# Optimization experiments

Hardware: AMD Instinct MI355X
Metric: run time of the kernel (lower is better)

Reference implementation:

```python
import jax, jax.numpy as jnp
import numpy as np


def _gcn_norm(edge_index, num_nodes, dtype):
    # PyG GCNConv.norm: add self-loops (weight 1), symmetric deg^{-1/2} normalization
    row, col = edge_index[0], edge_index[1]
    loop = jnp.arange(num_nodes, dtype=row.dtype)
    row = jnp.concatenate([row, loop])
    col = jnp.concatenate([col, loop])
    ew = jnp.ones(row.shape[0], dtype=dtype)
    deg = jax.ops.segment_sum(ew, row, num_segments=num_nodes)
    dis = jnp.where(deg > 0, jax.lax.rsqrt(deg), 0.0)
    norm = dis[row] * ew * dis[col]
    return row, col, norm


def _masked_gcn_conv(x, row, col, norm, sigma, W, b, num_nodes):
    # mask_features: edge gather -> diff/sigma -> square -> scatter-add -> exp mask
    h = (x[col] - x[row]) / sigma            # [E, F]
    h = norm[:, None] * h * h                # [E, F]
    mask = jax.ops.segment_sum(h, row, num_segments=num_nodes)        # [N, F]
    deg = jax.ops.segment_sum(jnp.ones_like(norm), row, num_segments=num_nodes)  # degree(source), >=1 due to self-loops
    x = x * jnp.exp(-mask / deg[:, None])
    # GCNConv: linear transform then normalized aggregation source->target
    xw = x @ W                               # [N, O]
    out = jax.ops.segment_sum(norm[:, None] * xw[row], col, num_segments=num_nodes)
    return out + b


def setup_inputs() -> dict:
    key = jax.random.key(0)
    ks = jax.random.split(key, 8)
    N, E, F, H, C = 100000, 1600000, 128, 64, 40
    g = 1.414  # xavier gain used for sigma
    return {
        "x": jax.random.normal(ks[0], (N, F), jnp.float32),
        "edge_index": jax.random.randint(ks[1], (2, E), 0, N, jnp.int64),
        "sigma1": jax.random.uniform(ks[2], (1, F), jnp.float32, -1.0, 1.0) * (g * np.sqrt(6.0 / (1 + F))),
        "W1": jax.random.normal(ks[3], (F, H), jnp.float32) * (1.0 / np.sqrt(F)),
        "b1": jnp.zeros((H,), jnp.float32),
        "sigma2": jax.random.uniform(ks[4], (1, H), jnp.float32, -1.0, 1.0) * (g * np.sqrt(6.0 / (1 + H))),
        "W2": jax.random.normal(ks[5], (H, C), jnp.float32) * (1.0 / np.sqrt(H)),
        "b2": jnp.zeros((C,), jnp.float32),
    }


def reference(x, edge_index, sigma1, W1, b1, sigma2, W2, b2):
    N = x.shape[0]
    row, col, norm = _gcn_norm(edge_index, N, x.dtype)
    x = _masked_gcn_conv(x, row, col, norm, sigma1, W1, b1, N)
    x = jax.nn.relu(x)
    # dropout is identity in eval mode
    x = _masked_gcn_conv(x, row, col, norm, sigma2, W2, b2, N)
    return jax.nn.log_softmax(x, axis=1)
```

## Files before the change

kernel.cpp:

```cpp
#include <hip/hip_runtime.h>
#include <cmath>

constexpr int F1 = 128;
constexpr int H  = 64;
constexpr int NC = 40;
constexpr int NXCD = 8;

constexpr int SCAN_TPB = 256;
constexpr int SCAN_IPT = 8;
constexpr int SCAN_EPB = SCAN_TPB * SCAN_IPT;

__device__ inline unsigned short f2bf(float f) {
    union { float f; unsigned u; } v; v.f = f;
    return (unsigned short)((v.u + 0x7FFFu + ((v.u >> 16) & 1u)) >> 16);
}
__device__ inline float bflo(unsigned p) { union { float f; unsigned u; } v; v.u = p << 16; return v.f; }
__device__ inline float bfhi(unsigned p) { union { float f; unsigned u; } v; v.u = p & 0xFFFF0000u; return v.f; }
__device__ inline void unpack8(uint4 raw, float* d) {
    d[0] = bflo(raw.x); d[1] = bfhi(raw.x); d[2] = bflo(raw.y); d[3] = bfhi(raw.y);
    d[4] = bflo(raw.z); d[5] = bfhi(raw.z); d[6] = bflo(raw.w); d[7] = bfhi(raw.w);
}

__global__ void isg_kernel(const float* __restrict__ s1, float* __restrict__ i1,
                           const float* __restrict__ s2, float* __restrict__ i2) {
    int i = threadIdx.x;
    if (i < F1) i1[i] = 1.0f / s1[i];
    if (i < H)  i2[i] = 1.0f / s2[i];
}

__global__ void prep_u_kernel(const float* __restrict__ x, const float* __restrict__ isg,
                              unsigned short* __restrict__ u, size_t n8, int F) {
    size_t idx = (size_t)blockIdx.x * blockDim.x + threadIdx.x;
    if (idx >= n8) return;
    size_t base = idx * 8;
    int fk = (int)(base % (size_t)F);
    float4 a0 = *(const float4*)&x[base];
    float4 a1 = *(const float4*)&x[base + 4];
    float4 s0 = *(const float4*)&isg[fk];
    float4 s1 = *(const float4*)&isg[fk + 4];
    uint4 p;
    p.x = (unsigned)f2bf(a0.x * s0.x) | ((unsigned)f2bf(a0.y * s0.y) << 16);
    p.y = (unsigned)f2bf(a0.z * s0.z) | ((unsigned)f2bf(a0.w * s0.w) << 16);
    p.z = (unsigned)f2bf(a1.x * s1.x) | ((unsigned)f2bf(a1.y * s1.y) << 16);
    p.w = (unsigned)f2bf(a1.z * s1.z) | ((unsigned)f2bf(a1.w * s1.w) << 16);
    *(uint4*)&u[base] = p;
}

__global__ void count8_kernel(const int* __restrict__ row, const int* __restrict__ col,
                              int* __restrict__ cntO, int* __restrict__ cntI,
                              int E, int chunk, int stride) {
    int p = blockIdx.x & (NXCD - 1);
    int gid = blockIdx.x >> 3;
    unsigned lo = (unsigned)(p * chunk);
    for (int e = gid * blockDim.x + threadIdx.x; e < E; e += stride) {
        int r = row[e], c = col[e];
        if ((unsigned)r - lo < (unsigned)chunk) atomicAdd(&cntO[r], 1);
        if ((unsigned)c - lo < (unsigned)chunk) atomicAdd(&cntI[c], 1);
    }
}

__global__ void scan_partial_kernel(const int* __restrict__ cnt, int* __restrict__ bsum, int M) {
    __shared__ int red[SCAN_TPB];
    int t = threadIdx.x;
    int i0 = blockIdx.x * SCAN_EPB + t * SCAN_IPT;
    int s = 0;
#pragma unroll
    for (int k = 0; k < SCAN_IPT; ++k) {
        int i = i0 + k;
        if (i < M) s += cnt[i];
    }
    red[t] = s;
    __syncthreads();
    for (int off = SCAN_TPB / 2; off > 0; off >>= 1) {
        if (t < off) red[t] += red[t + off];
        __syncthreads();
    }
    if (t == 0) bsum[blockIdx.x] = red[0];
}

__global__ void scan_offsets_kernel(int* __restrict__ bsum, int nb,
                                    int* __restrict__ rowptrO, int* __restrict__ rowptrI,
                                    int N, int E) {
    __shared__ int sh[1024];
    int t = threadIdx.x;
    sh[t] = (t < nb) ? bsum[t] : 0;
    __syncthreads();
    for (int off = 1; off < 1024; off <<= 1) {
        int v = (t >= off) ? sh[t - off] : 0;
        __syncthreads();
        sh[t] += v;
        __syncthreads();
    }
    if (t < nb) bsum[t] = (t > 0) ? sh[t - 1] : 0;
    if (t == 0) { rowptrO[N] = E; rowptrI[N] = E; }
}

__global__ void scan_final_kernel(int* __restrict__ cntO, int* __restrict__ cntI,
                                  const int* __restrict__ bsum,
                                  int* __restrict__ rowptrO, int* __restrict__ rowptrI,
                                  float* __restrict__ dis, int N, int E) {
    __shared__ int sh[SCAN_TPB];
    int t = threadIdx.x;
    int M = 2 * N;
    const int* cnt = cntO;
    int i0 = blockIdx.x * SCAN_EPB + t * SCAN_IPT;
    int cv[SCAN_IPT], pre[SCAN_IPT];
    int run = 0;
#pragma unroll
    for (int k = 0; k < SCAN_IPT; ++k) {
        int i = i0 + k;
        cv[k] = (i < M) ? cnt[i] : 0;
        pre[k] = run;
        run += cv[k];
    }
    sh[t] = run;
    __syncthreads();
    for (int off = 1; off < SCAN_TPB; off <<= 1) {
        int v = (t >= off) ? sh[t - off] : 0;
        __syncthreads();
        sh[t] += v;
        __syncthreads();
    }
    int toff = ((t > 0) ? sh[t - 1] : 0) + bsum[blockIdx.x];
#pragma unroll
    for (int k = 0; k < SCAN_IPT; ++k) {
        int i = i0 + k;
        if (i < M) {
            int val = toff + pre[k];
            if (i < N) {
                rowptrO[i] = val;
                cntO[i] = val;
                dis[i] = rsqrtf((float)(cv[k] + 1));
            } else {
                rowptrI[i - N] = val - E;
                cntI[i - N] = val - E;
            }
        }
    }
}

__global__ void build8_kernel(const int* __restrict__ row, const int* __restrict__ col,
                              int* __restrict__ curO, int* __restrict__ curI,
                              int* __restrict__ adjO, int* __restrict__ adjI,
                              int E, int chunk, int stride) {
    int p = blockIdx.x & (NXCD - 1);
    int gid = blockIdx.x >> 3;
    unsigned lo = (unsigned)(p * chunk);
    for (int e = gid * blockDim.x + threadIdx.x; e < E; e += stride) {
        int r = row[e], c = col[e];
        if ((unsigned)r - lo < (unsigned)chunk) adjO[atomicAdd(&curO[r], 1)] = c;
        if ((unsigned)c - lo < (unsigned)chunk) adjI[atomicAdd(&curI[c], 1)] = r;
    }
}

template<int F, int O, int R>
__global__ void fused_mask_gemm_kernel(const int* __restrict__ rowptr, const int* __restrict__ adj,
                                       const float* __restrict__ dis, const float* __restrict__ x,
                                       const unsigned short* __restrict__ u,
                                       const float* __restrict__ W,
                                       unsigned short* __restrict__ Ybf, int N) {
    constexpr int NT = R * 64;
    constexpr int G = F / 8;
    constexpr int NPI = 64 / G;
    constexpr int FP = F + 4;
    __shared__ __align__(16) float WsT[O * FP];
    __shared__ __align__(16) float Xs[R][FP];
    int tid = threadIdx.x;
    for (int i = tid; i < F * O; i += NT) {
        int f = i / O, o = i - f * O;
        WsT[o * FP + f] = W[i];
    }
    int w = tid >> 6, lane = tid & 63;
    int h = lane / G, j = lane % G;
    int r = blockIdx.x * R + w;
    if (r < N) {
        int beg = rowptr[r], end = rowptr[r + 1];
        float dr = dis[r];
        float inv_deg = 1.0f / (float)(end - beg + 1);
        float ur[8], acc[8];
        unpack8(*(const uint4*)&u[(size_t)r * F + 8 * j], ur);
#pragma unroll
        for (int k = 0; k < 8; ++k) acc[k] = 0.0f;
        for (int t = beg; t < end; t += NPI) {
            int e = t + h;
            bool valid = e < end;
            int c = adj[valid ? e : beg];
            float nrm = valid ? dr * dis[c] : 0.0f;
            float uc[8];
            unpack8(*(const uint4*)&u[(size_t)c * F + 8 * j], uc);
#pragma unroll
            for (int k = 0; k < 8; ++k) {
                float d = uc[k] - ur[k];
                acc[k] = fmaf(nrm * d, d, acc[k]);
            }
        }
#pragma unroll
        for (int off = G; off < 64; off <<= 1) {
#pragma unroll
            for (int k = 0; k < 8; ++k) acc[k] += __shfl_xor(acc[k], off);
        }
        if (h == 0) {
            float4 a0 = *(const float4*)&x[(size_t)r * F + 8 * j];
            float4 a1 = *(const float4*)&x[(size_t)r * F + 8 * j + 4];
            float xm[8] = {a0.x, a0.y, a0.z, a0.w, a1.x, a1.y, a1.z, a1.w};
#pragma unroll
            for (int k = 0; k < 8; ++k) xm[k] *= expf(-acc[k] * inv_deg);
            *(float4*)&Xs[w][8 * j]     = make_float4(xm[0], xm[1], xm[2], xm[3]);
            *(float4*)&Xs[w][8 * j + 4] = make_float4(xm[4], xm[5], xm[6], xm[7]);
        }
    }
    __syncthreads();
    if (r < N && lane < O) {
        float acc = 0.0f;
#pragma unroll
        for (int fq = 0; fq < F / 4; ++fq) {
            float4 xs = *(const float4*)&Xs[w][4 * fq];
            float4 ws = *(const float4*)&WsT[lane * FP + 4 * fq];
            acc = fmaf(xs.x, ws.x, acc); acc = fmaf(xs.y, ws.y, acc);
            acc = fmaf(xs.z, ws.z, acc); acc = fmaf(xs.w, ws.w, acc);
        }
        float other = __shfl_xor(acc, 1);
        if (!(lane & 1)) {
            unsigned p = (unsigned)f2bf(acc) | ((unsigned)f2bf(other) << 16);
            *(unsigned*)&Ybf[(size_t)r * O + lane] = p;
        }
    }
}

__global__ void agg_relu_kernel(const int* __restrict__ rowptr, const int* __restrict__ adj,
                                const float* __restrict__ dis, const unsigned short* __restrict__ ybf,
                                const float* __restrict__ bias, float* __restrict__ h1,
                                unsigned short* __restrict__ u2, const float* __restrict__ isg2, int N) {
    int c = blockIdx.x * (blockDim.x >> 6) + (threadIdx.x >> 6);
    if (c >= N) return;
    int lane = threadIdx.x & 63;
    int h = lane >> 3, j = lane & 7;
    int beg = rowptr[c], end = rowptr[c + 1];
    float dc = dis[c];
    float acc[8];
#pragma unroll
    for (int k = 0; k < 8; ++k) acc[k] = 0.0f;
    for (int t = beg; t < end; t += 8) {
        int e = t + h;
        bool valid = e < end;
        int rr = adj[valid ? e : beg];
        float nrm = valid ? dc * dis[rr] : 0.0f;
        float v[8];
        unpack8(*(const uint4*)&ybf[(size_t)rr * H + 8 * j], v);
#pragma unroll
        for (int k = 0; k < 8; ++k) acc[k] = fmaf(nrm, v[k], acc[k]);
    }
#pragma unroll
    for (int off = 8; off < 64; off <<= 1) {
#pragma unroll
        for (int k = 0; k < 8; ++k) acc[k] += __shfl_xor(acc[k], off);
    }
    if (h == 0) {
        float sv[8];
        unpack8(*(const uint4*)&ybf[(size_t)c * H + 8 * j], sv);
        float4 b0 = *(const float4*)&bias[8 * j];
        float4 b1v = *(const float4*)&bias[8 * j + 4];
        float bb[8] = {b0.x, b0.y, b0.z, b0.w, b1v.x, b1v.y, b1v.z, b1v.w};
        float4 s0 = *(const float4*)&isg2[8 * j];
        float4 s1 = *(const float4*)&isg2[8 * j + 4];
        float sg[8] = {s0.x, s0.y, s0.z, s0.w, s1.x, s1.y, s1.z, s1.w};
        float hv[8];
        float d2 = dc * dc;
#pragma unroll
        for (int k = 0; k < 8; ++k) hv[k] = fmaxf(fmaf(d2, sv[k], acc[k]) + bb[k], 0.0f);
        *(float4*)&h1[(size_t)c * H + 8 * j]     = make_float4(hv[0], hv[1], hv[2], hv[3]);
        *(float4*)&h1[(size_t)c * H + 8 * j + 4] = make_float4(hv[4], hv[5], hv[6], hv[7]);
        uint4 p;
        p.x = (unsigned)f2bf(hv[0] * sg[0]) | ((unsigned)f2bf(hv[1] * sg[1]) << 16);
        p.y = (unsigned)f2bf(hv[2] * sg[2]) | ((unsigned)f2bf(hv[3] * sg[3]) << 16);
        p.z = (unsigned)f2bf(hv[4] * sg[4]) | ((unsigned)f2bf(hv[5] * sg[5]) << 16);
        p.w = (unsigned)f2bf(hv[6] * sg[6]) | ((unsigned)f2bf(hv[7] * sg[7]) << 16);
        *(uint4*)&u2[(size_t)c * H + 8 * j] = p;
    }
}

__global__ void agg_lsm_kernel(const int* __restrict__ rowptr, const int* __restrict__ adj,
                               const float* __restrict__ dis, const unsigned short* __restrict__ ybf,
                               const float* __restrict__ bias, float* __restrict__ out, int N) {
    int c = blockIdx.x * (blockDim.x >> 6) + (threadIdx.x >> 6);
    if (c >= N) return;
    int lane = threadIdx.x & 63;
    int h = lane >> 4, j = lane & 15;
    bool active = j < 10;
    int beg = rowptr[c], end = rowptr[c + 1];
    float dc = dis[c];
    float a[4] = {0.f, 0.f, 0.f, 0.f};
    for (int t = beg; t < end; t += 4) {
        int e = t + h;
        bool valid = e < end;
        int rr = adj[valid ? e : beg];
        float nrm = (valid && active) ? dc * dis[rr] : 0.0f;
        uint2 raw = active ? *(const uint2*)&ybf[(size_t)rr * NC + 4 * j] : make_uint2(0u, 0u);
        a[0] = fmaf(nrm, bflo(raw.x), a[0]);
        a[1] = fmaf(nrm, bfhi(raw.x), a[1]);
        a[2] = fmaf(nrm, bflo(raw.y), a[2]);
        a[3] = fmaf(nrm, bfhi(raw.y), a[3]);
    }
#pragma unroll
    for (int off = 16; off < 64; off <<= 1) {
#pragma unroll
        for (int k = 0; k < 4; ++k) a[k] += __shfl_xor(a[k], off);
    }
    bool wr = (h == 0) && active;
    float v[4] = {-INFINITY, -INFINITY, -INFINITY, -INFINITY};
    if (wr) {
        uint2 sr = *(const uint2*)&ybf[(size_t)c * NC + 4 * j];
        float sv[4] = {bflo(sr.x), bfhi(sr.x), bflo(sr.y), bfhi(sr.y)};
        float4 bb = *(const float4*)&bias[4 * j];
        float b4[4] = {bb.x, bb.y, bb.z, bb.w};
        float d2 = dc * dc;
#pragma unroll
        for (int k = 0; k < 4; ++k) v[k] = fmaf(d2, sv[k], a[k]) + b4[k];
    }
    float m = fmaxf(fmaxf(v[0], v[1]), fmaxf(v[2], v[3]));
#pragma unroll
    for (int off = 8; off > 0; off >>= 1) m = fmaxf(m, __shfl_xor(m, off));
    float s = wr ? (expf(v[0] - m) + expf(v[1] - m) + expf(v[2] - m) + expf(v[3] - m)) : 0.0f;
#pragma unroll
    for (int off = 8; off > 0; off >>= 1) s += __shfl_xor(s, off);
    float mls = m + logf(s);
    if (wr)
        *(float4*)&out[(size_t)c * NC + 4 * j] = make_float4(v[0] - mls, v[1] - mls, v[2] - mls, v[3] - mls);
}

extern "C" void kernel_launch(void* const* d_in, const int* in_sizes, int n_in,
                              void* d_out, int out_size, void* d_ws, size_t ws_size,
                              hipStream_t stream) {
    const float* x    = (const float*)d_in[0];
    const int*   ei   = (const int*)  d_in[1];
    const float* sig1 = (const float*)d_in[2];
    const float* W1   = (const float*)d_in[3];
    const float* b1   = (const float*)d_in[4];
    const float* sig2 = (const float*)d_in[5];
    const float* W2   = (const float*)d_in[6];
    const float* b2   = (const float*)d_in[7];
    float* out = (float*)d_out;

    const int N = in_sizes[0] / F1;
    const int E = in_sizes[1] / 2;
    const int* row = ei;
    const int* col = ei + E;

    char* w = (char*)d_ws;
    auto alloc = [&](size_t bytes) { void* q = w; w += (bytes + 255) & ~255ull; return q; };
    int*   cntO    = (int*)  alloc((size_t)2 * N * 4);
    int*   cntI    = cntO + N;
    int*   rowptrO = (int*)  alloc((size_t)(N + 1) * 4);
    int*   rowptrI = (int*)  alloc((size_t)(N + 1) * 4);
    int*   adjO    = (int*)  alloc((size_t)E * 4);
    int*   adjI    = (int*)  alloc((size_t)E * 4);
    float* dis     = (float*)alloc((size_t)N * 4);
    float* isg1    = (float*)alloc(F1 * 4);
    float* isg2    = (float*)alloc(H * 4);
    int*   bsum    = (int*)  alloc(1024 * 4);
    unsigned short* u1   = (unsigned short*)alloc((size_t)N * F1 * 2);
    unsigned short* u2   = (unsigned short*)alloc((size_t)N * H * 2);
    unsigned short* ybf1 = (unsigned short*)alloc((size_t)N * H * 2);
    float* h1      = (float*)alloc((size_t)N * H * 4);
    unsigned short* ybf2 = u1;

    const int B = 256;
    const int chunk = (N + NXCD - 1) / NXCD;
    const int WPP = 1024;
    const int stride8 = WPP * B;
    dim3 g8(NXCD * WPP);
    const int M = 2 * N;
    const int nb = (M + SCAN_EPB - 1) / SCAN_EPB;

    hipMemsetAsync(cntO, 0, (size_t)2 * N * 4, stream);
    isg_kernel<<<1, 128, 0, stream>>>(sig1, isg1, sig2, isg2);
    prep_u_kernel<<<(int)(((size_t)N * F1 / 8 + B - 1) / B), B, 0, stream>>>(x, isg1, u1, (size_t)N * F1 / 8, F1);
    count8_kernel<<<g8, B, 0, stream>>>(row, col, cntO, cntI, E, chunk, stride8);
    scan_partial_kernel<<<nb, SCAN_TPB, 0, stream>>>(cntO, bsum, M);
    scan_offsets_kernel<<<1, 1024, 0, stream>>>(bsum, nb, rowptrO, rowptrI, N, E);
    scan_final_kernel<<<nb, SCAN_TPB, 0, stream>>>(cntO, cntI, bsum, rowptrO, rowptrI, dis, N, E);
    build8_kernel<<<g8, B, 0, stream>>>(row, col, cntO, cntI, adjO, adjI, E, chunk, stride8);

    fused_mask_gemm_kernel<F1, H, 8><<<(N + 7) / 8, 512, 0, stream>>>(rowptrO, adjO, dis, x, u1, W1, ybf1, N);
    agg_relu_kernel<<<(N + 3) / 4, B, 0, stream>>>(rowptrI, adjI, dis, ybf1, b1, h1, u2, isg2, N);

    fused_mask_gemm_kernel<H, NC, 8><<<(N + 7) / 8, 512, 0, stream>>>(rowptrO, adjO, dis, h1, u2, W2, ybf2, N);
    agg_lsm_kernel<<<(N + 3) / 4, B, 0, stream>>>(rowptrI, adjI, dis, ybf2, b2, out, N);
}
```

Before: 689.7 us.

## Batch neighbor gathers for memory parallelism and process two rows per wave in fused mask-GEMM

Each of the three gather loops now unrolls the neighbor walk so that several adjacency indices, dis values and feature rows are loaded before any arithmetic. This puts more independent global loads in flight per wave. The fused mask-GEMM kernel now handles two rows per wavefront (R=16 rows per 512-thread block). It keeps W untransposed in shared memory and reuses each W element for two output rows, which halves W staging per row. The cost is more registers per thread and an uneven split when row degrees differ.

```diff
diff --git a/kernel.cpp b/kernel.cpp
--- a/kernel.cpp
+++ b/kernel.cpp
@@ -159,70 +159,96 @@
                                        const unsigned short* __restrict__ u,
                                        const float* __restrict__ W,
                                        unsigned short* __restrict__ Ybf, int N) {
-    constexpr int NT = R * 64;
+    constexpr int NT = R * 32;
     constexpr int G = F / 8;
     constexpr int NPI = 64 / G;
-    constexpr int FP = F + 4;
-    __shared__ __align__(16) float WsT[O * FP];
-    __shared__ __align__(16) float Xs[R][FP];
+    constexpr int P = (NPI >= 8) ? 2 : 4;
+    __shared__ __align__(16) float Ws[F * O];
+    __shared__ __align__(16) float Xs[R][F];
     int tid = threadIdx.x;
-    for (int i = tid; i < F * O; i += NT) {
-        int f = i / O, o = i - f * O;
-        WsT[o * FP + f] = W[i];
-    }
+    for (int i = tid; i < F * O; i += NT) Ws[i] = W[i];
     int w = tid >> 6, lane = tid & 63;
     int h = lane / G, j = lane % G;
-    int r = blockIdx.x * R + w;
-    if (r < N) {
-        int beg = rowptr[r], end = rowptr[r + 1];
-        float dr = dis[r];
-        float inv_deg = 1.0f / (float)(end - beg + 1);
-        float ur[8], acc[8];
-        unpack8(*(const uint4*)&u[(size_t)r * F + 8 * j], ur);
-#pragma unroll
-        for (int k = 0; k < 8; ++k) acc[k] = 0.0f;
-        for (int t = beg; t < end; t += NPI) {
-            int e = t + h;
-            bool valid = e < end;
-            int c = adj[valid ? e : beg];
-            float nrm = valid ? dr * dis[c] : 0.0f;
-            float uc[8];
-            unpack8(*(const uint4*)&u[(size_t)c * F + 8 * j], uc);
-#pragma unroll
-            for (int k = 0; k < 8; ++k) {
-                float d = uc[k] - ur[k];
-                acc[k] = fmaf(nrm * d, d, acc[k]);
+    int base = blockIdx.x * R;
+#pragma unroll
+    for (int s = 0; s < 2; ++s) {
+        int r = base + 2 * w + s;
+        if (r < N) {
+            int beg = rowptr[r], end = rowptr[r + 1];
+            float dr = dis[r];
+            float inv_deg = 1.0f / (float)(end - beg + 1);
+            float ur[8], acc[8];
+            unpack8(*(const uint4*)&u[(size_t)r * F + 8 * j], ur);
+#pragma unroll
+            for (int k = 0; k < 8; ++k) acc[k] = 0.0f;
+            for (int t = beg; t < end; t += P * NPI) {
+                int cc[P]; float dd[P]; uint4 rw[P];
+#pragma unroll
+                for (int k = 0; k < P; ++k) {
+                    int e = t + k * NPI + h;
+                    cc[k] = adj[min(e, end - 1)];
+                }
+#pragma unroll
+                for (int k = 0; k < P; ++k) {
+                    int e = t + k * NPI + h;
+                    dd[k] = (e < end) ? dis[cc[k]] : 0.0f;
+                }
+#pragma unroll
+                for (int k = 0; k < P; ++k) rw[k] = *(const uint4*)&u[(size_t)cc[k] * F + 8 * j];
+#pragma unroll
+                for (int k = 0; k < P; ++k) {
+                    float nrm = dr * dd[k];
+                    float uc[8];
+                    unpack8(rw[k], uc);
+#pragma unroll
+                    for (int q = 0; q < 8; ++q) {
+                        float d = uc[q] - ur[q];
+                        acc[q] = fmaf(nrm * d, d, acc[q]);
+                    }
+                }
             }
-        }
-#pragma unroll
-        for (int off = G; off < 64; off <<= 1) {
-#pragma unroll
-            for (int k = 0; k < 8; ++k) acc[k] += __shfl_xor(acc[k], off);
-        }
-        if (h == 0) {
-            float4 a0 = *(const float4*)&x[(size_t)r * F + 8 * j];
-            float4 a1 = *(const float4*)&x[(size_t)r * F + 8 * j + 4];
-            float xm[8] = {a0.x, a0.y, a0.z, a0.w, a1.x, a1.y, a1.z, a1.w};
-#pragma unroll
-            for (int k = 0; k < 8; ++k) xm[k] *= expf(-acc[k] * inv_deg);
-            *(float4*)&Xs[w][8 * j]     = make_float4(xm[0], xm[1], xm[2], xm[3]);
-            *(float4*)&Xs[w][8 * j + 4] = make_float4(xm[4], xm[5], xm[6], xm[7]);
+#pragma unroll
+            for (int off = G; off < 64; off <<= 1) {
+#pragma unroll
+                for (int k = 0; k < 8; ++k) acc[k] += __shfl_xor(acc[k], off);
+            }
+            if (h == 0) {
+                float4 a0 = *(const float4*)&x[(size_t)r * F + 8 * j];
+                float4 a1 = *(const float4*)&x[(size_t)r * F + 8 * j + 4];
+                float xm[8] = {a0.x, a0.y, a0.z, a0.w, a1.x, a1.y, a1.z, a1.w};
+#pragma unroll
+                for (int k = 0; k < 8; ++k) xm[k] *= expf(-acc[k] * inv_deg);
+                *(float4*)&Xs[2 * w + s][8 * j]     = make_float4(xm[0], xm[1], xm[2], xm[3]);
+                *(float4*)&Xs[2 * w + s][8 * j + 4] = make_float4(xm[4], xm[5], xm[6], xm[7]);
+            }
         }
     }
     __syncthreads();
-    if (r < N && lane < O) {
-        float acc = 0.0f;
+    int r0 = base + 2 * w;
+    if (lane < O && r0 < N) {
+        bool two = (r0 + 1) < N;
+        float acc0 = 0.0f, acc1 = 0.0f;
 #pragma unroll
         for (int fq = 0; fq < F / 4; ++fq) {
-            float4 xs = *(const float4*)&Xs[w][4 * fq];
-            float4 ws = *(const float4*)&WsT[lane * FP + 4 * fq];
-            acc = fmaf(xs.x, ws.x, acc); acc = fmaf(xs.y, ws.y, acc);
-            acc = fmaf(xs.z, ws.z, acc); acc = fmaf(xs.w, ws.w, acc);
-        }
-        float other = __shfl_xor(acc, 1);
+            float4 x0 = *(const float4*)&Xs[2 * w][4 * fq];
+            float4 x1 = two ? *(const float4*)&Xs[2 * w + 1][4 * fq] : make_float4(0.f, 0.f, 0.f, 0.f);
+            float w0 = Ws[(4 * fq + 0) * O + lane];
+            float w1 = Ws[(4 * fq + 1) * O + lane];
+            float w2 = Ws[(4 * fq + 2) * O + lane];
+            float w3 = Ws[(4 * fq + 3) * O + lane];
+            acc0 = fmaf(x0.x, w0, acc0); acc1 = fmaf(x1.x, w0, acc1);
+            acc0 = fmaf(x0.y, w1, acc0); acc1 = fmaf(x1.y, w1, acc1);
+            acc0 = fmaf(x0.z, w2, acc0); acc1 = fmaf(x1.z, w2, acc1);
+            acc0 = fmaf(x0.w, w3, acc0); acc1 = fmaf(x1.w, w3, acc1);
+        }
+        float o0 = __shfl_xor(acc0, 1);
+        float o1 = __shfl_xor(acc1, 1);
         if (!(lane & 1)) {
-            unsigned p = (unsigned)f2bf(acc) | ((unsigned)f2bf(other) << 16);
-            *(unsigned*)&Ybf[(size_t)r * O + lane] = p;
+            *(unsigned*)&Ybf[(size_t)r0 * O + lane] =
+                (unsigned)f2bf(acc0) | ((unsigned)f2bf(o0) << 16);
+            if (two)
+                *(unsigned*)&Ybf[(size_t)(r0 + 1) * O + lane] =
+                    (unsigned)f2bf(acc1) | ((unsigned)f2bf(o1) << 16);
         }
     }
 }
@@ -240,15 +266,28 @@
     float acc[8];
 #pragma unroll
     for (int k = 0; k < 8; ++k) acc[k] = 0.0f;
-    for (int t = beg; t < end; t += 8) {
-        int e = t + h;
-        bool valid = e < end;
-        int rr = adj[valid ? e : beg];
-        float nrm = valid ? dc * dis[rr] : 0.0f;
-        float v[8];
-        unpack8(*(const uint4*)&ybf[(size_t)rr * H + 8 * j], v);
-#pragma unroll
-        for (int k = 0; k < 8; ++k) acc[k] = fmaf(nrm, v[k], acc[k]);
+    for (int t = beg; t < end; t += 16) {
+        int cc[2]; float dd[2]; uint4 rw[2];
+#pragma unroll
+        for (int k = 0; k < 2; ++k) {
+            int e = t + k * 8 + h;
+            cc[k] = adj[min(e, end - 1)];
+        }
+#pragma unroll
+        for (int k = 0; k < 2; ++k) {
+            int e = t + k * 8 + h;
+            dd[k] = (e < end) ? dis[cc[k]] : 0.0f;
+        }
+#pragma unroll
+        for (int k = 0; k < 2; ++k) rw[k] = *(const uint4*)&ybf[(size_t)cc[k] * H + 8 * j];
+#pragma unroll
+        for (int k = 0; k < 2; ++k) {
+            float nrm = dc * dd[k];
+            float v[8];
+            unpack8(rw[k], v);
+#pragma unroll
+            for (int q = 0; q < 8; ++q) acc[q] = fmaf(nrm, v[q], acc[q]);
+        }
     }
 #pragma unroll
     for (int off = 8; off < 64; off <<= 1) {
@@ -290,16 +329,29 @@
     int beg = rowptr[c], end = rowptr[c + 1];
     float dc = dis[c];
     float a[4] = {0.f, 0.f, 0.f, 0.f};
-    for (int t = beg; t < end; t += 4) {
-        int e = t + h;
-        bool valid = e < end;
-        int rr = adj[valid ? e : beg];
-        float nrm = (valid && active) ? dc * dis[rr] : 0.0f;
-        uint2 raw = active ? *(const uint2*)&ybf[(size_t)rr * NC + 4 * j] : make_uint2(0u, 0u);
-        a[0] = fmaf(nrm, bflo(raw.x), a[0]);
-        a[1] = fmaf(nrm, bfhi(raw.x), a[1]);
-        a[2] = fmaf(nrm, bflo(raw.y), a[2]);
-        a[3] = fmaf(nrm, bfhi(raw.y), a[3]);
+    for (int t = beg; t < end; t += 16) {
+        int cc[4]; float dd[4]; uint2 rw[4];
+#pragma unroll
+        for (int k = 0; k < 4; ++k) {
+            int e = t + k * 4 + h;
+            cc[k] = adj[min(e, end - 1)];
+        }
+#pragma unroll
+        for (int k = 0; k < 4; ++k) {
+            int e = t + k * 4 + h;
+            dd[k] = (e < end) ? dis[cc[k]] : 0.0f;
+        }
+#pragma unroll
+        for (int k = 0; k < 4; ++k)
+            rw[k] = active ? *(const uint2*)&ybf[(size_t)cc[k] * NC + 4 * j] : make_uint2(0u, 0u);
+#pragma unroll
+        for (int k = 0; k < 4; ++k) {
+            float nrm = dc * dd[k];
+            a[0] = fmaf(nrm, bflo(rw[k].x), a[0]);
+            a[1] = fmaf(nrm, bfhi(rw[k].x), a[1]);
+            a[2] = fmaf(nrm, bflo(rw[k].y), a[2]);
+            a[3] = fmaf(nrm, bfhi(rw[k].y), a[3]);
+        }
     }
 #pragma unroll
     for (int off = 16; off < 64; off <<= 1) {
@@ -381,9 +433,9 @@
     scan_final_kernel<<<nb, SCAN_TPB, 0, stream>>>(cntO, cntI, bsum, rowptrO, rowptrI, dis, N, E);
     build8_kernel<<<g8, B, 0, stream>>>(row, col, cntO, cntI, adjO, adjI, E, chunk, stride8);
 
-    fused_mask_gemm_kernel<F1, H, 8><<<(N + 7) / 8, 512, 0, stream>>>(rowptrO, adjO, dis, x, u1, W1, ybf1, N);
+    fused_mask_gemm_kernel<F1, H, 16><<<(N + 15) / 16, 512, 0, stream>>>(rowptrO, adjO, dis, x, u1, W1, ybf1, N);
     agg_relu_kernel<<<(N + 3) / 4, B, 0, stream>>>(rowptrI, adjI, dis, ybf1, b1, h1, u2, isg2, N);
 
-    fused_mask_gemm_kernel<H, NC, 8><<<(N + 7) / 8, 512, 0, stream>>>(rowptrO, adjO, dis, h1, u2, W2, ybf2, N);
+    fused_mask_gemm_kernel<H, NC, 16><<<(N + 15) / 16, 512, 0, stream>>>(rowptrO, adjO, dis, h1, u2, W2, ybf2, N);
     agg_lsm_kernel<<<(N + 3) / 4, B, 0, stream>>>(rowptrI, adjI, dis, ybf2, b2, out, N);
 }
```

Result: slower. 2.273 ms (+229.5%).
